# Performance work log

Measured on AMD Instinct MI355X. Metric: run time of the kernel, lower is better.

## Reference

```python
import jax, jax.numpy as jnp
import numpy as np

B, C, NP, PL = 1024, 3, 10, 100
D, H, L = 768, 12, 12
SF, TF = 56, 24
N = NP + 2
HD = D // H        # 64 per-head dim
D2 = HD // 2       # 32 rotary pairs
NMASK = 4          # max(1, int(0.4*10))
EPS = 1e-5


def _layernorm(x, g, b):
    m = jnp.mean(x, -1, keepdims=True)
    v = jnp.var(x, -1, keepdims=True)
    return (x - m) * jax.lax.rsqrt(v + EPS) * g + b


def _rope(x, cos, sin):
    # x: (B,H,N,HD) real; pairs are interleaved (even, odd) as in view_as_complex
    x2 = x.reshape(x.shape[:-1] + (D2, 2))
    xr, xi = x2[..., 0], x2[..., 1]
    outr = xr * cos - xi * sin
    outi = xr * sin + xi * cos
    return jnp.stack([outr, outi], axis=-1).reshape(x.shape)


def _forward(mask_idx, patches, stats, topo,
             patch_w, patch_b, stat_w, stat_b, topo_w, topo_b, mask_token,
             emb_g, emb_b,
             ln1_g, ln1_b, qkv_w, qkv_b, proj_w, proj_b,
             ln2_g, ln2_b, f1_w, f1_b, f2_w, f2_b,
             h1_w, h1_b, h2_w, h2_b):
    Bx = patches.shape[0]
    # (B,C,NP,PL) -> (B,NP,C*PL)
    flat_raw = jnp.transpose(patches, (0, 2, 1, 3)).reshape(Bx, NP, C * PL)
    targets = jax.lax.stop_gradient(flat_raw)
    patch_vec = flat_raw @ patch_w + patch_b                    # (B,NP,D)
    s = (stats @ stat_w + stat_b)[:, None, :]                   # (B,1,D)
    g = (topo @ topo_w + topo_b)[:, None, :]                    # (B,1,D)
    patch_vec = jnp.where(mask_idx[..., None], mask_token, patch_vec)
    tok = jnp.concatenate([patch_vec, s, g], axis=1)            # (B,N,D)
    tok = _layernorm(tok, emb_g, emb_b)

    # rotary tables for N tokens
    freq = 1.0 / (10000.0 ** (jnp.arange(0, HD, 2, dtype=jnp.float32) / HD))
    ang = jnp.arange(N, dtype=jnp.float32)[:, None] * freq[None, :]  # (N,D2)
    cos, sin = jnp.cos(ang), jnp.sin(ang)
    scale = 1.0 / jnp.sqrt(jnp.float32(HD))

    def step(x, p):
        l1g, l1b, qw, qb, pw, pb, l2g, l2b, w1, b1, w2, b2 = p
        h = _layernorm(x, l1g, l1b)
        qkv = (h @ qw + qb).reshape(Bx, N, 3, H, HD)
        q = jnp.transpose(qkv[:, :, 0], (0, 2, 1, 3))           # (B,H,N,HD)
        k = jnp.transpose(qkv[:, :, 1], (0, 2, 1, 3))
        v = jnp.transpose(qkv[:, :, 2], (0, 2, 1, 3))
        q = _rope(q, cos, sin)
        k = _rope(k, cos, sin)
        attn = jax.nn.softmax(jnp.einsum('bhqd,bhkd->bhqk', q, k) * scale, axis=-1)
        out = jnp.einsum('bhqk,bhkd->bhqd', attn, v)
        out = jnp.transpose(out, (0, 2, 1, 3)).reshape(Bx, N, D)
        x = x + out @ pw + pb
        h = _layernorm(x, l2g, l2b)
        x = x + jnp.maximum(h @ w1 + b1, 0.0) @ w2 + b2
        return x, None

    x, _ = jax.lax.scan(step, tok, (ln1_g, ln1_b, qkv_w, qkv_b, proj_w, proj_b,
                                    ln2_g, ln2_b, f1_w, f1_b, f2_w, f2_b))

    token_out = x[:, :NP, :]
    pred = jnp.maximum(token_out @ h1_w + h1_b, 0.0) @ h2_w + h2_b  # (B,NP,C*PL)
    se = jnp.where(mask_idx[..., None], (pred - targets) ** 2, 0.0)
    denom = jnp.sum(mask_idx).astype(jnp.float32) * jnp.float32(C * PL)
    return jnp.sum(se) / denom


def setup_inputs():
    key = jax.random.key(0)
    ks = jax.random.split(key, 40)
    s = 0.02
    inp = {
        'patches': jax.random.normal(ks[0], (B, C, NP, PL), jnp.float32),
        'stats': jax.random.normal(ks[1], (B, SF), jnp.float32),
        'topo': jax.random.normal(ks[2], (B, TF), jnp.float32),
    }
    # exactly NMASK masked positions per row
    scores = jax.random.uniform(ks[3], (B, NP))
    idx = jnp.argsort(scores, axis=1)[:, :NMASK]
    inp['mask_idx'] = jnp.zeros((B, NP), bool).at[jnp.arange(B)[:, None], idx].set(True)
    rn = lambda k, sh: jax.random.normal(k, sh, jnp.float32) * s
    inp.update({
        'patch_w': rn(ks[4], (C * PL, D)), 'patch_b': jnp.zeros((D,)),
        'stat_w': rn(ks[5], (SF, D)), 'stat_b': jnp.zeros((D,)),
        'topo_w': rn(ks[6], (TF, D)), 'topo_b': jnp.zeros((D,)),
        'mask_token': rn(ks[7], (D,)),
        'emb_g': jnp.ones((D,)), 'emb_b': jnp.zeros((D,)),
        'ln1_g': jnp.ones((L, D)), 'ln1_b': jnp.zeros((L, D)),
        'qkv_w': rn(ks[8], (L, D, 3 * D)), 'qkv_b': jnp.zeros((L, 3 * D)),
        'proj_w': rn(ks[9], (L, D, D)), 'proj_b': jnp.zeros((L, D)),
        'ln2_g': jnp.ones((L, D)), 'ln2_b': jnp.zeros((L, D)),
        'f1_w': rn(ks[10], (L, D, 2 * D)), 'f1_b': jnp.zeros((L, 2 * D)),
        'f2_w': rn(ks[11], (L, 2 * D, D)), 'f2_b': jnp.zeros((L, D)),
        'h1_w': rn(ks[12], (D, D)), 'h1_b': jnp.zeros((D,)),
        'h2_w': rn(ks[13], (D, C * PL)), 'h2_b': jnp.zeros((C * PL,)),
    })
    return inp


def reference(patches, stats, topo, mask_idx,
              patch_w, patch_b, stat_w, stat_b, topo_w, topo_b, mask_token,
              emb_g, emb_b,
              ln1_g, ln1_b, qkv_w, qkv_b, proj_w, proj_b,
              ln2_g, ln2_b, f1_w, f1_b, f2_w, f2_b,
              h1_w, h1_b, h2_w, h2_b):
    return _forward(mask_idx, patches, stats, topo,
                    patch_w, patch_b, stat_w, stat_b, topo_w, topo_b, mask_token,
                    emb_g, emb_b, ln1_g, ln1_b, qkv_w, qkv_b, proj_w, proj_b,
                    ln2_g, ln2_b, f1_w, f1_b, f2_w, f2_b,
                    h1_w, h1_b, h2_w, h2_b)
```

## Files before the change

### kernel.cpp

```cpp
#include <hip/hip_runtime.h>
#include <hip/hip_bf16.h>
#include <cstddef>

#define B_   1024
#define C_   3
#define NP_  10
#define PL_  100
#define D_   768
#define H_   12
#define L_   12
#define N_   12
#define HD_  64

typedef __attribute__((ext_vector_type(8))) short short8;
typedef __attribute__((ext_vector_type(4))) float float4v;

__device__ __forceinline__ ushort f2bf(float x) {
    __hip_bfloat16 h = __float2bfloat16(x);
    return *(ushort*)&h;
}
__device__ __forceinline__ float bf2f(ushort u) {
    union { unsigned u32; float f; } x; x.u32 = ((unsigned)u) << 16; return x.f;
}

__device__ __forceinline__ void block_reduce2(float& a, float& b) {
    __shared__ float sa[4], sb[4];
#pragma unroll
    for (int off = 32; off > 0; off >>= 1) {
        a += __shfl_down(a, off);
        b += __shfl_down(b, off);
    }
    int wid = threadIdx.x >> 6, lane = threadIdx.x & 63;
    __syncthreads();
    if (lane == 0) { sa[wid] = a; sb[wid] = b; }
    __syncthreads();
    if (threadIdx.x == 0) {
        float ta = 0.f, tb = 0.f;
#pragma unroll
        for (int i = 0; i < 4; ++i) { ta += sa[i]; tb += sb[i]; }
        sa[0] = ta; sb[0] = tb;
    }
    __syncthreads();
    a = sa[0]; b = sb[0];
}

#define BM 64
#define BN 64
#define BK 16

__global__ __launch_bounds__(256) void gemm_kernel(
    const float* __restrict__ A, const float* __restrict__ W,
    const float* __restrict__ bias, const float* __restrict__ res,
    float* __restrict__ C, int M, int N, int K, int amode, int relu)
{
    __shared__ float As[BK][BM];
    __shared__ float Ws[BK][BN];

    const int tid = threadIdx.x;
    const int tx = tid & 15, ty = tid >> 4;
    const int m0 = blockIdx.y * BM, n0 = blockIdx.x * BN;

    float acc[4][4] = {};

    const int am  = tid & 63;
    const int akq = tid >> 6;
    const int wn  = (tid & 15) * 4;
    const int wk  = tid >> 4;

    for (int k0 = 0; k0 < K; k0 += BK) {
        float4 av = make_float4(0.f, 0.f, 0.f, 0.f);
        int gm = m0 + am;
        int gk = k0 + akq * 4;
        if (gm < M && gk < K) {
            if (amode == 0) {
                av = *(const float4*)(A + (size_t)gm * K + gk);
            } else {
                int bb = gm / 10, n = gm % 10, c = gk / 100, p = gk % 100;
                av = *(const float4*)(A + (size_t)(((bb * 3 + c) * 10 + n) * 100 + p));
            }
        }
        As[akq * 4 + 0][am] = av.x;
        As[akq * 4 + 1][am] = av.y;
        As[akq * 4 + 2][am] = av.z;
        As[akq * 4 + 3][am] = av.w;

        float4 wv = make_float4(0.f, 0.f, 0.f, 0.f);
        int gkw = k0 + wk, gn = n0 + wn;
        if (gkw < K && gn < N)
            wv = *(const float4*)(W + (size_t)gkw * N + gn);
        *(float4*)&Ws[wk][wn] = wv;

        __syncthreads();

#pragma unroll
        for (int kk = 0; kk < BK; ++kk) {
            float4 a = *(const float4*)&As[kk][ty * 4];
            float4 b = *(const float4*)&Ws[kk][tx * 4];
            acc[0][0] += a.x * b.x; acc[0][1] += a.x * b.y; acc[0][2] += a.x * b.z; acc[0][3] += a.x * b.w;
            acc[1][0] += a.y * b.x; acc[1][1] += a.y * b.y; acc[1][2] += a.y * b.z; acc[1][3] += a.y * b.w;
            acc[2][0] += a.z * b.x; acc[2][1] += a.z * b.y; acc[2][2] += a.z * b.z; acc[2][3] += a.z * b.w;
            acc[3][0] += a.w * b.x; acc[3][1] += a.w * b.y; acc[3][2] += a.w * b.z; acc[3][3] += a.w * b.w;
        }
        __syncthreads();
    }

#pragma unroll
    for (int i = 0; i < 4; ++i) {
        int row = m0 + ty * 4 + i;
        if (row >= M) continue;
#pragma unroll
        for (int j = 0; j < 4; ++j) {
            int col = n0 + tx * 4 + j;
            if (col >= N) continue;
            float v = acc[i][j] + bias[col];
            if (relu) v = fmaxf(v, 0.f);
            if (res) v += res[(size_t)row * N + col];
            C[(size_t)row * N + col] = v;
        }
    }
}

__global__ __launch_bounds__(256) void transpose_bf16(
    const float* __restrict__ in, ushort* __restrict__ out, int K, int N)
{
    __shared__ float t[32][33];
    const int tx = threadIdx.x & 31, ty = threadIdx.x >> 5;
    const int k0 = blockIdx.y * 32, n0 = blockIdx.x * 32;
#pragma unroll
    for (int i = 0; i < 4; ++i) {
        int k = k0 + ty + i * 8, n = n0 + tx;
        t[ty + i * 8][tx] = (k < K && n < N) ? in[(size_t)k * N + n] : 0.f;
    }
    __syncthreads();
#pragma unroll
    for (int i = 0; i < 4; ++i) {
        int n = n0 + ty + i * 8, k = k0 + tx;
        if (n < N && k < K)
            out[(size_t)n * K + k] = f2bf(t[tx][ty + i * 8]);
    }
}

#define LDT 40

__global__ __launch_bounds__(256) void mfma_gemm(
    const ushort* __restrict__ A, const ushort* __restrict__ Wt,
    const float* __restrict__ bias, const float* __restrict__ res,
    void* __restrict__ outp, int M, int N, int K, int relu, int obf16)
{
    __shared__ ushort As[128 * LDT];
    __shared__ ushort Bs[128 * LDT];

    const int tid = threadIdx.x;
    const int m0 = blockIdx.y * 128, n0 = blockIdx.x * 128;
    const int lane = tid & 63, w = tid >> 6;
    const int wm = (w & 1) * 64, wn = (w >> 1) * 64;
    const int quad = lane >> 4, l16 = lane & 15;

    const int srow = tid >> 1, scol = (tid & 1) * 16;

    float4v acc[4][4] = {};

    for (int k0 = 0; k0 < K; k0 += 32) {
        {
            const ushort* src = A + (size_t)(m0 + srow) * K + k0 + scol;
            *(short8*)(As + srow * LDT + scol)     = *(const short8*)(src);
            *(short8*)(As + srow * LDT + scol + 8) = *(const short8*)(src + 8);
        }
        {
            int n = n0 + srow;
            short8 v0, v1;
            if (n < N) {
                const ushort* src = Wt + (size_t)n * K + k0 + scol;
                v0 = *(const short8*)(src);
                v1 = *(const short8*)(src + 8);
            } else {
#pragma unroll
                for (int i = 0; i < 8; ++i) { v0[i] = 0; v1[i] = 0; }
            }
            *(short8*)(Bs + srow * LDT + scol)     = v0;
            *(short8*)(Bs + srow * LDT + scol + 8) = v1;
        }
        __syncthreads();

        short8 af[4], bfr[4];
#pragma unroll
        for (int i = 0; i < 4; ++i) {
            af[i]  = *(const short8*)(As + (wm + i * 16 + l16) * LDT + quad * 8);
            bfr[i] = *(const short8*)(Bs + (wn + i * 16 + l16) * LDT + quad * 8);
        }
#pragma unroll
        for (int mi = 0; mi < 4; ++mi)
#pragma unroll
            for (int ni = 0; ni < 4; ++ni)
                acc[mi][ni] = __builtin_amdgcn_mfma_f32_16x16x32_bf16(
                    af[mi], bfr[ni], acc[mi][ni], 0, 0, 0);
        __syncthreads();
    }

    float* outf = (float*)outp;
    ushort* outb = (ushort*)outp;
#pragma unroll
    for (int mi = 0; mi < 4; ++mi) {
#pragma unroll
        for (int ni = 0; ni < 4; ++ni) {
            int col = n0 + wn + ni * 16 + l16;
            if (col >= N) continue;
            float bv = bias[col];
#pragma unroll
            for (int r = 0; r < 4; ++r) {
                int row = m0 + wm + mi * 16 + quad * 4 + r;
                float v = acc[mi][ni][r] + bv;
                if (relu) v = fmaxf(v, 0.f);
                size_t o = (size_t)row * N + col;
                if (res) v += res[o];
                if (obf16) outb[o] = f2bf(v);
                else       outf[o] = v;
            }
        }
    }
}

__global__ __launch_bounds__(256) void ln_kernel(
    const float* __restrict__ X, const float* __restrict__ g,
    const float* __restrict__ b, ushort* __restrict__ O)
{
    const int row = blockIdx.x;
    const int t = threadIdx.x;
    const float* x = X + (size_t)row * D_;
    float v0 = x[t], v1 = x[t + 256], v2 = x[t + 512];
    float s  = v0 + v1 + v2;
    float ss = v0 * v0 + v1 * v1 + v2 * v2;
    block_reduce2(s, ss);
    float mean = s * (1.f / D_);
    float var  = ss * (1.f / D_) - mean * mean;
    float rstd = rsqrtf(var + 1e-5f);
    ushort* o = O + (size_t)row * D_;
    o[t]       = f2bf((v0 - mean) * rstd * g[t]       + b[t]);
    o[t + 256] = f2bf((v1 - mean) * rstd * g[t + 256] + b[t + 256]);
    o[t + 512] = f2bf((v2 - mean) * rstd * g[t + 512] + b[t + 512]);
}

__global__ __launch_bounds__(256) void assemble_ln_kernel(
    const float* __restrict__ pvec, const float* __restrict__ svec,
    const float* __restrict__ gvec, const int* __restrict__ mask,
    const float* __restrict__ mtok, const float* __restrict__ g,
    const float* __restrict__ b, float* __restrict__ O)
{
    const int row = blockIdx.x;
    const int bb = row / N_, n = row % N_;
    const int t = threadIdx.x;
    float v0, v1, v2;
    if (n < NP_) {
        if (mask[bb * NP_ + n]) {
            v0 = mtok[t]; v1 = mtok[t + 256]; v2 = mtok[t + 512];
        } else {
            const float* p = pvec + (size_t)(bb * NP_ + n) * D_;
            v0 = p[t]; v1 = p[t + 256]; v2 = p[t + 512];
        }
    } else if (n == NP_) {
        const float* p = svec + (size_t)bb * D_;
        v0 = p[t]; v1 = p[t + 256]; v2 = p[t + 512];
    } else {
        const float* p = gvec + (size_t)bb * D_;
        v0 = p[t]; v1 = p[t + 256]; v2 = p[t + 512];
    }
    float s  = v0 + v1 + v2;
    float ss = v0 * v0 + v1 * v1 + v2 * v2;
    block_reduce2(s, ss);
    float mean = s * (1.f / D_);
    float var  = ss * (1.f / D_) - mean * mean;
    float rstd = rsqrtf(var + 1e-5f);
    float* o = O + (size_t)row * D_;
    o[t]       = (v0 - mean) * rstd * g[t]       + b[t];
    o[t + 256] = (v1 - mean) * rstd * g[t + 256] + b[t + 256];
    o[t + 512] = (v2 - mean) * rstd * g[t + 512] + b[t + 512];
}

__global__ __launch_bounds__(64) void attn_kernel(
    const ushort* __restrict__ QKV, ushort* __restrict__ OUT)
{
    const int bh = blockIdx.x;
    const int bb = bh / H_, h = bh % H_;
    const int t = threadIdx.x;

    __shared__ float q[N_][HD_], k[N_][HD_], v[N_][HD_], p[N_][N_];

    const ushort* base = QKV + (size_t)bb * N_ * (3 * D_) + h * HD_;
#pragma unroll
    for (int n = 0; n < N_; ++n) {
        q[n][t] = bf2f(base[n * (3 * D_) + t]);
        k[n][t] = bf2f(base[n * (3 * D_) + D_ + t]);
        v[n][t] = bf2f(base[n * (3 * D_) + 2 * D_ + t]);
    }
    __syncthreads();

    if (t < 32) {
        float freq = exp2f(-(float)t * (13.287712379549449f / 32.0f));
#pragma unroll
        for (int n = 0; n < N_; ++n) {
            float ang = (float)n * freq;
            float sn, cs;
            sincosf(ang, &sn, &cs);
            float xr = q[n][2 * t], xi = q[n][2 * t + 1];
            q[n][2 * t]     = xr * cs - xi * sn;
            q[n][2 * t + 1] = xr * sn + xi * cs;
            xr = k[n][2 * t]; xi = k[n][2 * t + 1];
            k[n][2 * t]     = xr * cs - xi * sn;
            k[n][2 * t + 1] = xr * sn + xi * cs;
        }
    }
    __syncthreads();

    for (int idx = t; idx < N_ * N_; idx += 64) {
        int i = idx / N_, j = idx % N_;
        float s = 0.f;
#pragma unroll
        for (int d = 0; d < HD_; ++d) s += q[i][d] * k[j][d];
        p[i][j] = s * 0.125f;
    }
    __syncthreads();

    if (t < N_) {
        float mx = -1e30f;
#pragma unroll
        for (int j = 0; j < N_; ++j) mx = fmaxf(mx, p[t][j]);
        float e[N_], sum = 0.f;
#pragma unroll
        for (int j = 0; j < N_; ++j) { e[j] = expf(p[t][j] - mx); sum += e[j]; }
        float inv = 1.f / sum;
#pragma unroll
        for (int j = 0; j < N_; ++j) p[t][j] = e[j] * inv;
    }
    __syncthreads();

#pragma unroll
    for (int i = 0; i < N_; ++i) {
        float o = 0.f;
#pragma unroll
        for (int j = 0; j < N_; ++j) o += p[i][j] * v[j][t];
        OUT[((size_t)bb * N_ + i) * D_ + h * HD_ + t] = f2bf(o);
    }
}

__global__ __launch_bounds__(256) void tokensel_kernel(
    const float* __restrict__ X, ushort* __restrict__ XS)
{
    const int r = blockIdx.x;
    const int c = blockIdx.y * 256 + threadIdx.x;
    XS[(size_t)r * D_ + c] =
        f2bf(X[(size_t)((r / 10) * 12 + (r % 10)) * D_ + c]);
}

__global__ __launch_bounds__(256) void loss_partial_kernel(
    const float* __restrict__ pred, const float* __restrict__ patches,
    const int* __restrict__ mask, float* __restrict__ part)
{
    const int row = blockIdx.x;
    const int t = threadIdx.x;
    if (!mask[row]) {
        if (t == 0) part[row] = 0.f;
        return;
    }
    const int bb = row / NP_, n = row % NP_;
    float s = 0.f;
    for (int kk = t; kk < C_ * PL_; kk += 256) {
        int c = kk / PL_, pp = kk % PL_;
        float tgt = patches[((size_t)(bb * C_ + c) * NP_ + n) * PL_ + pp];
        float d = pred[(size_t)row * (C_ * PL_) + kk] - tgt;
        s += d * d;
    }
    float dummy = 0.f;
    block_reduce2(s, dummy);
    if (t == 0) part[row] = s;
}

__global__ __launch_bounds__(256) void loss_final_kernel(
    const float* __restrict__ part, const int* __restrict__ mask,
    float* __restrict__ out)
{
    const int t = threadIdx.x;
    float s = 0.f, cnt = 0.f;
    for (int i = t; i < B_ * NP_; i += 256) {
        s += part[i];
        cnt += (float)mask[i];
    }
    block_reduce2(s, cnt);
    if (t == 0) out[0] = s / (cnt * (float)(C_ * PL_));
}

extern "C" void kernel_launch(void* const* d_in, const int* in_sizes, int n_in,
                              void* d_out, int out_size, void* d_ws, size_t ws_size,
                              hipStream_t stream) {
    const float* patches = (const float*)d_in[0];
    const float* stats   = (const float*)d_in[1];
    const float* topo    = (const float*)d_in[2];
    const int*   mask    = (const int*)d_in[3];
    const float* patch_w = (const float*)d_in[4];
    const float* patch_b = (const float*)d_in[5];
    const float* stat_w  = (const float*)d_in[6];
    const float* stat_b  = (const float*)d_in[7];
    const float* topo_w  = (const float*)d_in[8];
    const float* topo_b  = (const float*)d_in[9];
    const float* mtok    = (const float*)d_in[10];
    const float* emb_g   = (const float*)d_in[11];
    const float* emb_b   = (const float*)d_in[12];
    const float* ln1_g   = (const float*)d_in[13];
    const float* ln1_b   = (const float*)d_in[14];
    const float* qkv_w   = (const float*)d_in[15];
    const float* qkv_b   = (const float*)d_in[16];
    const float* proj_w  = (const float*)d_in[17];
    const float* proj_b  = (const float*)d_in[18];
    const float* ln2_g   = (const float*)d_in[19];
    const float* ln2_b   = (const float*)d_in[20];
    const float* f1_w    = (const float*)d_in[21];
    const float* f1_b    = (const float*)d_in[22];
    const float* f2_w    = (const float*)d_in[23];
    const float* f2_b    = (const float*)d_in[24];
    const float* h1_w    = (const float*)d_in[25];
    const float* h1_b    = (const float*)d_in[26];
    const float* h2_w    = (const float*)d_in[27];
    const float* h2_b    = (const float*)d_in[28];

    const size_t XSZ = (size_t)B_ * N_ * D_;
    float*  X    = (float*)d_ws;
    ushort* HB   = (ushort*)(X + XSZ);
    ushort* BIGS = HB + XSZ;
    float*  PART = (float*)(BIGS + (size_t)B_ * N_ * 3 * D_);
    ushort* WB   = (ushort*)(PART + (size_t)B_ * NP_);

    ushort* qkvT  = WB;
    ushort* projT = qkvT + (size_t)L_ * 3 * D_ * D_;
    ushort* f1T   = projT + (size_t)L_ * D_ * D_;
    ushort* f2T   = f1T + (size_t)L_ * 2 * D_ * D_;
    ushort* h1T   = f2T + (size_t)L_ * 2 * D_ * D_;
    ushort* h2T   = h1T + (size_t)D_ * D_;

    ushort* QKV  = BIGS;
    float*  PVEC = (float*)BIGS;
    float*  SVEC = PVEC + (size_t)B_ * NP_ * D_;
    float*  GVEC = SVEC + (size_t)B_ * D_;
    ushort* MID  = BIGS;
    float*  PRED = (float*)BIGS;
    ushort* XS   = BIGS + (size_t)2 * B_ * NP_ * 300;
    ushort* PMID = XS + (size_t)B_ * NP_ * D_;

    const dim3 blk(256);

    for (int l = 0; l < L_; ++l) {
        transpose_bf16<<<dim3(2304 / 32, 768 / 32), blk, 0, stream>>>(
            qkv_w + (size_t)l * D_ * 3 * D_, qkvT + (size_t)l * 3 * D_ * D_, D_, 3 * D_);
        transpose_bf16<<<dim3(768 / 32, 768 / 32), blk, 0, stream>>>(
            proj_w + (size_t)l * D_ * D_, projT + (size_t)l * D_ * D_, D_, D_);
        transpose_bf16<<<dim3(1536 / 32, 768 / 32), blk, 0, stream>>>(
            f1_w + (size_t)l * D_ * 2 * D_, f1T + (size_t)l * 2 * D_ * D_, D_, 2 * D_);
        transpose_bf16<<<dim3(768 / 32, 1536 / 32), blk, 0, stream>>>(
            f2_w + (size_t)l * 2 * D_ * D_, f2T + (size_t)l * 2 * D_ * D_, 2 * D_, D_);
    }
    transpose_bf16<<<dim3(768 / 32, 768 / 32), blk, 0, stream>>>(h1_w, h1T, D_, D_);
    transpose_bf16<<<dim3(10, 768 / 32), blk, 0, stream>>>(h2_w, h2T, D_, C_ * PL_);

    gemm_kernel<<<dim3(D_ / 64, (B_ * NP_) / 64), blk, 0, stream>>>(
        patches, patch_w, patch_b, nullptr, PVEC, B_ * NP_, D_, C_ * PL_, 2, 0);
    gemm_kernel<<<dim3(D_ / 64, B_ / 64), blk, 0, stream>>>(
        stats, stat_w, stat_b, nullptr, SVEC, B_, D_, 56, 0, 0);
    gemm_kernel<<<dim3(D_ / 64, B_ / 64), blk, 0, stream>>>(
        topo, topo_w, topo_b, nullptr, GVEC, B_, D_, 24, 0, 0);
    assemble_ln_kernel<<<B_ * N_, blk, 0, stream>>>(
        PVEC, SVEC, GVEC, mask, mtok, emb_g, emb_b, X);

    for (int l = 0; l < L_; ++l) {
        ln_kernel<<<B_ * N_, blk, 0, stream>>>(X, ln1_g + l * D_, ln1_b + l * D_, HB);
        mfma_gemm<<<dim3(18, 96), blk, 0, stream>>>(
            HB, qkvT + (size_t)l * 3 * D_ * D_, qkv_b + l * 3 * D_, nullptr, QKV,
            B_ * N_, 3 * D_, D_, 0, 1);
        attn_kernel<<<B_ * H_, dim3(64), 0, stream>>>(QKV, HB);
        mfma_gemm<<<dim3(6, 96), blk, 0, stream>>>(
            HB, projT + (size_t)l * D_ * D_, proj_b + l * D_, X, X,
            B_ * N_, D_, D_, 0, 0);
        ln_kernel<<<B_ * N_, blk, 0, stream>>>(X, ln2_g + l * D_, ln2_b + l * D_, HB);
        mfma_gemm<<<dim3(12, 96), blk, 0, stream>>>(
            HB, f1T + (size_t)l * 2 * D_ * D_, f1_b + l * 2 * D_, nullptr, MID,
            B_ * N_, 2 * D_, D_, 1, 1);
        mfma_gemm<<<dim3(6, 96), blk, 0, stream>>>(
            MID, f2T + (size_t)l * 2 * D_ * D_, f2_b + l * D_, X, X,
            B_ * N_, D_, 2 * D_, 0, 0);
    }

    tokensel_kernel<<<dim3(B_ * NP_, 3), blk, 0, stream>>>(X, XS);
    mfma_gemm<<<dim3(6, 80), blk, 0, stream>>>(
        XS, h1T, h1_b, nullptr, PMID, B_ * NP_, D_, D_, 1, 1);
    mfma_gemm<<<dim3(3, 80), blk, 0, stream>>>(
        PMID, h2T, h2_b, nullptr, PRED, B_ * NP_, C_ * PL_, D_, 0, 0);
    loss_partial_kernel<<<B_ * NP_, blk, 0, stream>>>(PRED, patches, mask, PART);
    loss_final_kernel<<<1, blk, 0, stream>>>(PART, mask, (float*)d_out);
}
```

Before: 5.266 ms.

## Use async global-to-LDS loads in MFMA GEMM and batch weight transposes

The MFMA GEMM now stages A and B tiles with global_load_lds 16-byte async copies into an unpadded LDS layout instead of register round-trips into padded tiles. This removes per-thread register staging, but the unpadded stride may add LDS bank conflicts. The per-layer weight transpose launches are merged into one z-batched launch per weight type, cutting launch overhead. The patch-embedding projection moves from the fp32 SIMT GEMM to the bf16 MFMA GEMM, using a gather kernel and K padded to 320, which trades fp32 precision for tensor-core throughput.

```diff
diff --git a/kernel.cpp b/kernel.cpp
--- a/kernel.cpp
+++ b/kernel.cpp
@@ -23,6 +23,12 @@
     union { unsigned u32; float f; } x; x.u32 = ((unsigned)u) << 16; return x.f;
 }
 
+__device__ __forceinline__ void async_cp16(const ushort* g, ushort* lds) {
+    __builtin_amdgcn_global_load_lds(
+        (const __attribute__((address_space(1))) unsigned int*)g,
+        (__attribute__((address_space(3))) unsigned int*)lds, 16, 0, 0);
+}
+
 __device__ __forceinline__ void block_reduce2(float& a, float& b) {
     __shared__ float sa[4], sb[4];
 #pragma unroll
@@ -50,8 +56,8 @@
 
 __global__ __launch_bounds__(256) void gemm_kernel(
     const float* __restrict__ A, const float* __restrict__ W,
-    const float* __restrict__ bias, const float* __restrict__ res,
-    float* __restrict__ C, int M, int N, int K, int amode, int relu)
+    const float* __restrict__ bias, float* __restrict__ C,
+    int M, int N, int K)
 {
     __shared__ float As[BK][BM];
     __shared__ float Ws[BK][BN];
@@ -71,13 +77,13 @@
         float4 av = make_float4(0.f, 0.f, 0.f, 0.f);
         int gm = m0 + am;
         int gk = k0 + akq * 4;
-        if (gm < M && gk < K) {
-            if (amode == 0) {
-                av = *(const float4*)(A + (size_t)gm * K + gk);
-            } else {
-                int bb = gm / 10, n = gm % 10, c = gk / 100, p = gk % 100;
-                av = *(const float4*)(A + (size_t)(((bb * 3 + c) * 10 + n) * 100 + p));
-            }
+        if (gm < M && gk + 3 < K)
+            av = *(const float4*)(A + (size_t)gm * K + gk);
+        else if (gm < M) {
+            float tmp[4] = {0.f, 0.f, 0.f, 0.f};
+            for (int i = 0; i < 4; ++i)
+                if (gk + i < K) tmp[i] = A[(size_t)gm * K + gk + i];
+            av = make_float4(tmp[0], tmp[1], tmp[2], tmp[3]);
         }
         As[akq * 4 + 0][am] = av.x;
         As[akq * 4 + 1][am] = av.y;
@@ -112,43 +118,54 @@
         for (int j = 0; j < 4; ++j) {
             int col = n0 + tx * 4 + j;
             if (col >= N) continue;
-            float v = acc[i][j] + bias[col];
-            if (relu) v = fmaxf(v, 0.f);
-            if (res) v += res[(size_t)row * N + col];
-            C[(size_t)row * N + col] = v;
-        }
-    }
-}
-
-__global__ __launch_bounds__(256) void transpose_bf16(
-    const float* __restrict__ in, ushort* __restrict__ out, int K, int N)
+            C[(size_t)row * N + col] = acc[i][j] + bias[col];
+        }
+    }
+}
+
+__global__ __launch_bounds__(256) void transpose_bf16_b(
+    const float* __restrict__ in, ushort* __restrict__ out,
+    int K, int N, int Kpad, int Npad, size_t in_stride, size_t out_stride)
 {
     __shared__ float t[32][33];
+    const float* inz = in + (size_t)blockIdx.z * in_stride;
+    ushort* outz = out + (size_t)blockIdx.z * out_stride;
     const int tx = threadIdx.x & 31, ty = threadIdx.x >> 5;
     const int k0 = blockIdx.y * 32, n0 = blockIdx.x * 32;
 #pragma unroll
     for (int i = 0; i < 4; ++i) {
         int k = k0 + ty + i * 8, n = n0 + tx;
-        t[ty + i * 8][tx] = (k < K && n < N) ? in[(size_t)k * N + n] : 0.f;
+        t[ty + i * 8][tx] = (k < K && n < N) ? inz[(size_t)k * N + n] : 0.f;
     }
     __syncthreads();
 #pragma unroll
     for (int i = 0; i < 4; ++i) {
         int n = n0 + ty + i * 8, k = k0 + tx;
-        if (n < N && k < K)
-            out[(size_t)n * K + k] = f2bf(t[tx][ty + i * 8]);
-    }
-}
-
-#define LDT 40
+        if (n < Npad && k < Kpad)
+            outz[(size_t)n * Kpad + k] = f2bf(t[tx][ty + i * 8]);
+    }
+}
+
+__global__ __launch_bounds__(256) void patch_gather(
+    const float* __restrict__ patches, ushort* __restrict__ PB)
+{
+    int idx = blockIdx.x * 256 + threadIdx.x;
+    int row = idx / 320, col = idx % 320;
+    ushort v = 0;
+    if (col < 300) {
+        int bb = row / 10, n = row % 10, c = col / 100, p = col % 100;
+        v = f2bf(patches[(size_t)((bb * 3 + c) * 10 + n) * 100 + p]);
+    }
+    PB[idx] = v;
+}
 
 __global__ __launch_bounds__(256) void mfma_gemm(
     const ushort* __restrict__ A, const ushort* __restrict__ Wt,
     const float* __restrict__ bias, const float* __restrict__ res,
     void* __restrict__ outp, int M, int N, int K, int relu, int obf16)
 {
-    __shared__ ushort As[128 * LDT];
-    __shared__ ushort Bs[128 * LDT];
+    __shared__ ushort As[128 * 32];
+    __shared__ ushort Bs[128 * 32];
 
     const int tid = threadIdx.x;
     const int m0 = blockIdx.y * 128, n0 = blockIdx.x * 128;
@@ -156,37 +173,32 @@
     const int wm = (w & 1) * 64, wn = (w >> 1) * 64;
     const int quad = lane >> 4, l16 = lane & 15;
 
-    const int srow = tid >> 1, scol = (tid & 1) * 16;
+    const int srow = (w << 4) + (lane >> 2);
+    const int scol = (lane & 3) << 3;
+    const size_t arow0 = (size_t)(m0 + srow) * K;
+    const size_t arow1 = arow0 + (size_t)64 * K;
+    const size_t brow0 = (size_t)(n0 + srow) * K;
+    const size_t brow1 = brow0 + (size_t)64 * K;
+    ushort* AsW0 = As + (w << 9);
+    ushort* AsW1 = As + 2048 + (w << 9);
+    ushort* BsW0 = Bs + (w << 9);
+    ushort* BsW1 = Bs + 2048 + (w << 9);
 
     float4v acc[4][4] = {};
 
     for (int k0 = 0; k0 < K; k0 += 32) {
-        {
-            const ushort* src = A + (size_t)(m0 + srow) * K + k0 + scol;
-            *(short8*)(As + srow * LDT + scol)     = *(const short8*)(src);
-            *(short8*)(As + srow * LDT + scol + 8) = *(const short8*)(src + 8);
-        }
-        {
-            int n = n0 + srow;
-            short8 v0, v1;
-            if (n < N) {
-                const ushort* src = Wt + (size_t)n * K + k0 + scol;
-                v0 = *(const short8*)(src);
-                v1 = *(const short8*)(src + 8);
-            } else {
-#pragma unroll
-                for (int i = 0; i < 8; ++i) { v0[i] = 0; v1[i] = 0; }
-            }
-            *(short8*)(Bs + srow * LDT + scol)     = v0;
-            *(short8*)(Bs + srow * LDT + scol + 8) = v1;
-        }
+        const int kc = k0 + scol;
+        async_cp16(A + arow0 + kc, AsW0);
+        async_cp16(A + arow1 + kc, AsW1);
+        async_cp16(Wt + brow0 + kc, BsW0);
+        async_cp16(Wt + brow1 + kc, BsW1);
         __syncthreads();
 
         short8 af[4], bfr[4];
 #pragma unroll
         for (int i = 0; i < 4; ++i) {
-            af[i]  = *(const short8*)(As + (wm + i * 16 + l16) * LDT + quad * 8);
-            bfr[i] = *(const short8*)(Bs + (wn + i * 16 + l16) * LDT + quad * 8);
+            af[i]  = *(const short8*)(As + (wm + i * 16 + l16) * 32 + quad * 8);
+            bfr[i] = *(const short8*)(Bs + (wn + i * 16 + l16) * 32 + quad * 8);
         }
 #pragma unroll
         for (int mi = 0; mi < 4; ++mi)
@@ -434,11 +446,13 @@
     ushort* f2T   = f1T + (size_t)L_ * 2 * D_ * D_;
     ushort* h1T   = f2T + (size_t)L_ * 2 * D_ * D_;
     ushort* h2T   = h1T + (size_t)D_ * D_;
+    ushort* pwT   = h2T + (size_t)384 * D_;
 
     ushort* QKV  = BIGS;
     float*  PVEC = (float*)BIGS;
     float*  SVEC = PVEC + (size_t)B_ * NP_ * D_;
     float*  GVEC = SVEC + (size_t)B_ * D_;
+    ushort* PB   = (ushort*)(GVEC + (size_t)B_ * D_);
     ushort* MID  = BIGS;
     float*  PRED = (float*)BIGS;
     ushort* XS   = BIGS + (size_t)2 * B_ * NP_ * 300;
@@ -446,25 +460,28 @@
 
     const dim3 blk(256);
 
-    for (int l = 0; l < L_; ++l) {
-        transpose_bf16<<<dim3(2304 / 32, 768 / 32), blk, 0, stream>>>(
-            qkv_w + (size_t)l * D_ * 3 * D_, qkvT + (size_t)l * 3 * D_ * D_, D_, 3 * D_);
-        transpose_bf16<<<dim3(768 / 32, 768 / 32), blk, 0, stream>>>(
-            proj_w + (size_t)l * D_ * D_, projT + (size_t)l * D_ * D_, D_, D_);
-        transpose_bf16<<<dim3(1536 / 32, 768 / 32), blk, 0, stream>>>(
-            f1_w + (size_t)l * D_ * 2 * D_, f1T + (size_t)l * 2 * D_ * D_, D_, 2 * D_);
-        transpose_bf16<<<dim3(768 / 32, 1536 / 32), blk, 0, stream>>>(
-            f2_w + (size_t)l * 2 * D_ * D_, f2T + (size_t)l * 2 * D_ * D_, 2 * D_, D_);
-    }
-    transpose_bf16<<<dim3(768 / 32, 768 / 32), blk, 0, stream>>>(h1_w, h1T, D_, D_);
-    transpose_bf16<<<dim3(10, 768 / 32), blk, 0, stream>>>(h2_w, h2T, D_, C_ * PL_);
-
-    gemm_kernel<<<dim3(D_ / 64, (B_ * NP_) / 64), blk, 0, stream>>>(
-        patches, patch_w, patch_b, nullptr, PVEC, B_ * NP_, D_, C_ * PL_, 2, 0);
+    transpose_bf16_b<<<dim3(72, 24, L_), blk, 0, stream>>>(
+        qkv_w, qkvT, D_, 3 * D_, D_, 3 * D_, (size_t)D_ * 3 * D_, (size_t)3 * D_ * D_);
+    transpose_bf16_b<<<dim3(24, 24, L_), blk, 0, stream>>>(
+        proj_w, projT, D_, D_, D_, D_, (size_t)D_ * D_, (size_t)D_ * D_);
+    transpose_bf16_b<<<dim3(48, 24, L_), blk, 0, stream>>>(
+        f1_w, f1T, D_, 2 * D_, D_, 2 * D_, (size_t)D_ * 2 * D_, (size_t)2 * D_ * D_);
+    transpose_bf16_b<<<dim3(24, 48, L_), blk, 0, stream>>>(
+        f2_w, f2T, 2 * D_, D_, 2 * D_, D_, (size_t)2 * D_ * D_, (size_t)2 * D_ * D_);
+    transpose_bf16_b<<<dim3(24, 24, 1), blk, 0, stream>>>(
+        h1_w, h1T, D_, D_, D_, D_, 0, 0);
+    transpose_bf16_b<<<dim3(12, 24, 1), blk, 0, stream>>>(
+        h2_w, h2T, D_, 300, D_, 384, 0, 0);
+    transpose_bf16_b<<<dim3(24, 10, 1), blk, 0, stream>>>(
+        patch_w, pwT, 300, D_, 320, D_, 0, 0);
+
+    patch_gather<<<(B_ * NP_ * 320) / 256, blk, 0, stream>>>(patches, PB);
+    mfma_gemm<<<dim3(6, 80), blk, 0, stream>>>(
+        PB, pwT, patch_b, nullptr, PVEC, B_ * NP_, D_, 320, 0, 0);
     gemm_kernel<<<dim3(D_ / 64, B_ / 64), blk, 0, stream>>>(
-        stats, stat_w, stat_b, nullptr, SVEC, B_, D_, 56, 0, 0);
+        stats, stat_w, stat_b, SVEC, B_, D_, 56);
     gemm_kernel<<<dim3(D_ / 64, B_ / 64), blk, 0, stream>>>(
-        topo, topo_w, topo_b, nullptr, GVEC, B_, D_, 24, 0, 0);
+        topo, topo_w, topo_b, GVEC, B_, D_, 24);
     assemble_ln_kernel<<<B_ * N_, blk, 0, stream>>>(
         PVEC, SVEC, GVEC, mask, mtok, emb_g, emb_b, X);
 
```

After: 4.714 ms. -10.5%, faster.
